# Performance work log

Measured on AMD Instinct MI355X. Metric: run time of the kernel, lower is better.

The kernel has to match this reference:

```python
import jax, jax.numpy as jnp
import numpy as np

B = 65536          # bs * m
N_NODES = 2        # fixed by module usage (job-machine pair graphs)
IN_FEAT = 256
N_HEADS = 4
N_HIDDEN = 256     # concat=False -> n_hidden = out_features
SLOPE = 0.2


def setup_inputs() -> dict:
    key = jax.random.key(0)
    k_h, k_adj, k_w, k_a = jax.random.split(key, 4)
    h = jax.random.normal(k_h, (B, N_NODES, IN_FEAT), dtype=jnp.float32)
    # adjacency: ij=1 means edge j->i; force self-loops on the diagonal
    adj = jax.random.randint(k_adj, (B, 1, N_NODES, N_NODES), 0, 2, dtype=jnp.int32)
    diag = jnp.arange(N_NODES)
    adj = adj.at[..., diag, diag].set(1)
    # xavier-normal-ish scales
    W = jax.random.normal(k_w, (IN_FEAT, N_HIDDEN * N_HEADS), dtype=jnp.float32) * (2.0 / (IN_FEAT + N_HIDDEN * N_HEADS)) ** 0.5
    a = jax.random.normal(k_a, (N_HEADS, 2 * N_HIDDEN, 1), dtype=jnp.float32) * (2.0 / (2 * N_HIDDEN + 1)) ** 0.5
    return {"h": h, "adj_mat": adj, "W": W, "a": a}


def reference(h, adj_mat, W, a):
    # h: (B, N, F_in); W: (F_in, H*D); a: (H, 2D, 1); adj_mat: (B, 1, N, N)
    Bsz, n_nodes, _ = h.shape
    n_heads = a.shape[0]
    n_hidden = a.shape[1] // 2
    # (B, N, H*D) -> (B, H, N, D)
    ht = (h @ W).reshape(Bsz, n_nodes, n_heads, n_hidden).transpose(0, 2, 1, 3)
    # attention scores: e[b,h,i,j] = leakyrelu(src[b,h,i] + tgt[b,h,j])
    src = jnp.einsum('bhnd,hd->bhn', ht, a[:, :n_hidden, 0])
    tgt = jnp.einsum('bhnd,hd->bhn', ht, a[:, n_hidden:, 0])
    e = jax.nn.leaky_relu(src[..., :, None] + tgt[..., None, :], SLOPE)
    e = jnp.where(adj_mat > 0, e, -jnp.inf)  # (B, H, N, N)
    attn = jax.nn.softmax(e, axis=-1)
    h_prime = jnp.einsum('bhij,bhjd->bhid', attn, ht)  # (B, H, N, D)
    # concat=False -> mean over heads
    return h_prime.mean(axis=1)  # (B, N, D)
```

## Files before the change

kernel.cpp:

```cpp
#include <hip/hip_runtime.h>
#include <hip/hip_bf16.h>


typedef __attribute__((ext_vector_type(8))) short short8;
typedef __attribute__((ext_vector_type(4))) float floatx4;

__device__ __forceinline__ float bf2f(short u) {
    union { unsigned int i; float f; } v;
    v.i = ((unsigned int)(unsigned short)u) << 16;
    return v.f;
}
__device__ __forceinline__ unsigned int pk2(float lo, float hi) {
    __hip_bfloat162 t = __float22bfloat162_rn(make_float2(lo, hi));
    union { __hip_bfloat162 h; unsigned int u; } cv; cv.h = t;
    return cv.u;
}

__global__ void gat_prep(const float* __restrict__ W, const float* __restrict__ a,
                         __hip_bfloat16* __restrict__ PT,
                         __hip_bfloat16* __restrict__ Wt2) {
    int b = blockIdx.x;
    if (b < 1024) {
        int idx = b * 256 + threadIdx.x;
        int d = idx & 255, hh = (idx >> 8) & 3, k = idx >> 10;
        int j = k >> 5, kl = k & 31;
        Wt2[(((hh * 8 + j) * 256 + d) << 5) + kl] =
            __float2bfloat16(W[k * 1024 + hh * 256 + d]);
    } else {
        int wid = (b - 1024) * 4 + (threadIdx.x >> 6);
        int lane = threadIdx.x & 63;
        int k = wid & 255, h = (wid >> 8) & 3, half = wid >> 10;
        float4 wv = *(const float4*)(W + k * 1024 + h * 256 + lane * 4);
        float4 av = *(const float4*)(a + h * 512 + half * 256 + lane * 4);
        float s = wv.x * av.x + wv.y * av.y + wv.z * av.z + wv.w * av.w;
        #pragma unroll
        for (int off = 32; off; off >>= 1) s += __shfl_down(s, off);
        if (lane == 0) PT[(half * 4 + h) * 256 + k] = __float2bfloat16(s);
        if (lane == 1) PT[2048 + wid] = __float2bfloat16(0.f);
    }
}

#define TB 32
#define ROWS 64

__global__ __launch_bounds__(256, 3)
void gat_main(const float* __restrict__ hin,
              const int* __restrict__ adj,
              const __hip_bfloat16* __restrict__ PT,
              const __hip_bfloat16* __restrict__ Wt2,
              float* __restrict__ out) {
    __shared__ __align__(16) short sH[ROWS * 256];
    __shared__ __align__(16) short sZd[2][ROWS * 64];
    __shared__ __align__(16) float2 sC[TB * 4 * 2];
    float (*sS)[16] = (float (*)[16])(&sZd[1][0]);

    const int tid = threadIdx.x;
    const int lane = tid & 63;
    const int wave = tid >> 6;
    const int m = lane & 15;
    const int q = lane >> 4;
    const long batch0 = (long)blockIdx.x * TB;
    char* sHb = (char*)sH;
    char* sZb = (char*)sZd;

    short8 ptf[8];
    {
        const short* ptg = (const short*)PT;
        #pragma unroll
        for (int ks = 0; ks < 8; ++ks)
            ptf[ks] = *(const short8*)(ptg + m * 256 + ks * 32 + q * 8);
    }
    int4 av = ((const int4*)adj)[batch0 + (tid >> 3)];

    {
        const float4* gh = (const float4*)(hin + batch0 * 512);
        #pragma unroll
        for (int it = 0; it < 16; ++it) {
            int idx = tid + it * 256;
            int r = idx >> 6, c4 = idx & 63;
            float4 v = gh[idx];
            uint2 bv;
            bv.x = pk2(v.x, v.y);
            bv.y = pk2(v.z, v.w);
            *(uint2*)(sHb + r * 512 + ((c4 * 8) ^ ((r & 7) << 4))) = bv;
        }
    }
    __syncthreads();

    {
        int row = wave * 16 + m;
        floatx4 a0 = {0.f, 0.f, 0.f, 0.f};
        #pragma unroll
        for (int ks = 0; ks < 8; ++ks) {
            short8 f0 = *(const short8*)(sHb + row * 512 +
                          ((ks * 64 + q * 16) ^ ((row & 7) << 4)));
            a0 = __builtin_amdgcn_mfma_f32_16x16x32_bf16(f0, ptf[ks], a0, 0, 0, 0);
        }
        #pragma unroll
        for (int r = 0; r < 4; ++r)
            sS[wave * 16 + q * 4 + r][m] = a0[r];
    }
    __syncthreads();

    {
        int lb = tid >> 3, hh = (tid >> 1) & 3, i = tid & 1;
        int m0 = i ? av.z : av.x, m1 = i ? av.w : av.y;
        float s  = sS[lb * 2 + i][hh];
        float t0 = sS[lb * 2][4 + hh], t1 = sS[lb * 2 + 1][4 + hh];
        float e0 = s + t0; e0 = e0 >= 0.f ? e0 : 0.2f * e0;
        float e1 = s + t1; e1 = e1 >= 0.f ? e1 : 0.2f * e1;
        e0 = fminf(fmaxf(e0, -80.f), 80.f);
        e1 = fminf(fmaxf(e1, -80.f), 80.f);
        bool k0 = m0 > 0, k1 = m1 > 0;
        float f0 = k0 ? e0 : -1e30f, f1 = k1 ? e1 : -1e30f;
        float mx = fmaxf(f0, f1);
        float p0 = k0 ? __expf(e0 - mx) : 0.f;
        float p1 = k1 ? __expf(e1 - mx) : 0.f;
        float den = p0 + p1;
        float inv = den > 1e-30f ? 0.25f / den : 0.f;
        sC[(lb * 4 + hh) * 2 + i] = make_float2(p0 * inv, p1 * inv);
    }
    __syncthreads();

    const int zg = tid & 7, zrb = tid >> 3;

    #define ZBUILD(ch, buf)                                                     \
    {                                                                           \
        int hh_ = (ch) >> 2, kc_ = (ch) & 3;                                    \
        _Pragma("unroll")                                                       \
        for (int half = 0; half < 2; ++half) {                                  \
            int zr = zrb + half * 32;                                           \
            float2 c = sC[((zr >> 1) * 4 + hh_) * 2 + (zr & 1)];                \
            int hr = zr & ~1;                                                   \
            int co = kc_ * 128 + zg * 16;                                       \
            short8 v0 = *(const short8*)(sHb + hr * 512 + (co ^ ((hr & 7) << 4))); \
            short8 v1 = *(const short8*)(sHb + (hr + 1) * 512 + (co ^ (((hr + 1) & 7) << 4))); \
            int4 zv; int* zp = (int*)&zv;                                       \
            _Pragma("unroll")                                                   \
            for (int jj = 0; jj < 4; ++jj) {                                    \
                float z0 = c.x * bf2f(v0[jj * 2])     + c.y * bf2f(v1[jj * 2]); \
                float z1 = c.x * bf2f(v0[jj * 2 + 1]) + c.y * bf2f(v1[jj * 2 + 1]); \
                zp[jj] = (int)pk2(z0, z1);                                      \
            }                                                                   \
            *(int4*)(sZb + (buf) * 8192 + zr * 128 + ((zg * 16) ^ ((zr & 7) << 4))) = zv; \
        }                                                                       \
    }

    floatx4 acc[4][4];
    #pragma unroll
    for (int i = 0; i < 4; ++i)
        #pragma unroll
        for (int j = 0; j < 4; ++j)
            acc[i][j] = (floatx4){0.f, 0.f, 0.f, 0.f};

    ZBUILD(0, 0);
    __syncthreads();

    int cur = 0;
    #pragma unroll 1
    for (int ch = 0; ch < 16; ++ch) {
        short8 bfr[2][4];
        {
            int hh = ch >> 2, kc = ch & 3;
            #pragma unroll
            for (int ks = 0; ks < 2; ++ks) {
                const short* wb = (const short*)Wt2 +
                    (((hh * 8 + kc * 2 + ks) * 256 + wave * 64 + m) << 5) + q * 8;
                #pragma unroll
                for (int nt = 0; nt < 4; ++nt)
                    bfr[ks][nt] = *(const short8*)(wb + (nt << 9));
            }
        }
        if (ch < 15) ZBUILD(ch + 1, cur ^ 1);
        #pragma unroll
        for (int ks = 0; ks < 2; ++ks)
            #pragma unroll
            for (int mt = 0; mt < 4; ++mt) {
                int row = mt * 16 + m;
                short8 af = *(const short8*)(sZb + cur * 8192 + row * 128 +
                              ((ks * 64 + q * 16) ^ ((row & 7) << 4)));
                #pragma unroll
                for (int nt = 0; nt < 4; ++nt)
                    acc[mt][nt] = __builtin_amdgcn_mfma_f32_16x16x32_bf16(
                        af, bfr[ks][nt], acc[mt][nt], 0, 0, 0);
            }
        __syncthreads();
        cur ^= 1;
    }

    {
        float* og = out + batch0 * 512;
        #pragma unroll
        for (int mt = 0; mt < 4; ++mt)
            #pragma unroll
            for (int nt = 0; nt < 4; ++nt) {
                int col = wave * 64 + nt * 16 + m;
                #pragma unroll
                for (int r = 0; r < 4; ++r)
                    og[(mt * 16 + q * 4 + r) * 256 + col] = acc[mt][nt][r];
            }
    }
    #undef ZBUILD
}

extern "C" void kernel_launch(void* const* d_in, const int* in_sizes, int n_in,
                              void* d_out, int out_size, void* d_ws, size_t ws_size,
                              hipStream_t stream) {
    const float* hin = (const float*)d_in[0];
    const int* adj   = (const int*)d_in[1];
    const float* W   = (const float*)d_in[2];
    const float* a   = (const float*)d_in[3];
    float* out       = (float*)d_out;

    __hip_bfloat16* PT  = (__hip_bfloat16*)d_ws;
    __hip_bfloat16* Wt2 = PT + 16 * 256;

    if (ws_size < (16 * 256 + 256 * 1024) * sizeof(__hip_bfloat16)) return;

    int B = in_sizes[0] / 512;
    gat_prep<<<1536, 256, 0, stream>>>(W, a, PT, Wt2);
    gat_main<<<B / TB, 256, 0, stream>>>(hin, adj, PT, Wt2, out);
}
```

Before: 291.3 us.

## Unroll main loop by two with register double-buffered weight fragments and lighter barriers

Unrolls the 16-chunk MFMA loop by two so the weight B-fragments for the next chunk are loaded into a second register set while the current chunk's MFMAs run, making the global-load latency overlap compute. The ping-pong LDS buffer index becomes a compile-time constant. __syncthreads is replaced with an explicit lgkmcnt wait plus s_barrier, which avoids waiting on outstanding global (vmcnt) loads at each barrier. Holding a second set of 8 short8 fragments raises register pressure under launch_bounds(256,3), which could cause spills or lower occupancy.

After: 342.5 us. +17.6%, slower.

```diff
diff --git a/kernel.cpp b/kernel.cpp
--- a/kernel.cpp
+++ b/kernel.cpp
@@ -62,6 +62,7 @@
     const long batch0 = (long)blockIdx.x * TB;
     char* sHb = (char*)sH;
     char* sZb = (char*)sZd;
+    const short* w2s = (const short*)Wt2;
 
     short8 ptf[8];
     {
@@ -146,6 +147,40 @@
         }                                                                       \
     }
 
+    #define LOADB(bfr, ch)                                                      \
+    {                                                                           \
+        int hh_ = (ch) >> 2, kc_ = (ch) & 3;                                    \
+        _Pragma("unroll")                                                       \
+        for (int ks = 0; ks < 2; ++ks) {                                        \
+            const short* wb = w2s +                                             \
+                (((hh_ * 8 + kc_ * 2 + ks) * 256 + wave * 64 + m) << 5) + q * 8;\
+            _Pragma("unroll")                                                   \
+            for (int nt = 0; nt < 4; ++nt)                                      \
+                bfr[ks * 4 + nt] = *(const short8*)(wb + (nt << 9));            \
+        }                                                                       \
+    }
+
+    #define MMASTEP(bfr, BUF)                                                   \
+    {                                                                           \
+        _Pragma("unroll")                                                       \
+        for (int ks = 0; ks < 2; ++ks)                                          \
+            _Pragma("unroll")                                                   \
+            for (int mt = 0; mt < 4; ++mt) {                                    \
+                int row = mt * 16 + m;                                          \
+                short8 af = *(const short8*)(sZb + (BUF) * 8192 + row * 128 +   \
+                              ((ks * 64 + q * 16) ^ ((row & 7) << 4)));         \
+                _Pragma("unroll")                                               \
+                for (int nt = 0; nt < 4; ++nt)                                  \
+                    acc[mt][nt] = __builtin_amdgcn_mfma_f32_16x16x32_bf16(      \
+                        af, bfr[ks * 4 + nt], acc[mt][nt], 0, 0, 0);            \
+            }                                                                   \
+    }
+
+    #define LOOPBAR()                                                           \
+        asm volatile("s_waitcnt lgkmcnt(0)" ::: "memory");                      \
+        __builtin_amdgcn_s_barrier();                                           \
+        asm volatile("" ::: "memory");
+
     floatx4 acc[4][4];
     #pragma unroll
     for (int i = 0; i < 4; ++i)
@@ -153,39 +188,25 @@
         for (int j = 0; j < 4; ++j)
             acc[i][j] = (floatx4){0.f, 0.f, 0.f, 0.f};
 
+    short8 bfrA[8], bfrB[8];
+
+    LOADB(bfrA, 0);
     ZBUILD(0, 0);
     __syncthreads();
 
-    int cur = 0;
     #pragma unroll 1
-    for (int ch = 0; ch < 16; ++ch) {
-        short8 bfr[2][4];
-        {
-            int hh = ch >> 2, kc = ch & 3;
-            #pragma unroll
-            for (int ks = 0; ks < 2; ++ks) {
-                const short* wb = (const short*)Wt2 +
-                    (((hh * 8 + kc * 2 + ks) * 256 + wave * 64 + m) << 5) + q * 8;
-                #pragma unroll
-                for (int nt = 0; nt < 4; ++nt)
-                    bfr[ks][nt] = *(const short8*)(wb + (nt << 9));
-            }
+    for (int ch2 = 0; ch2 < 8; ++ch2) {
+        int ch = ch2 * 2;
+        LOADB(bfrB, ch + 1);
+        ZBUILD(ch + 1, 1);
+        MMASTEP(bfrA, 0);
+        LOOPBAR();
+        if (ch2 < 7) {
+            LOADB(bfrA, ch + 2);
+            ZBUILD(ch + 2, 0);
         }
-        if (ch < 15) ZBUILD(ch + 1, cur ^ 1);
-        #pragma unroll
-        for (int ks = 0; ks < 2; ++ks)
-            #pragma unroll
-            for (int mt = 0; mt < 4; ++mt) {
-                int row = mt * 16 + m;
-                short8 af = *(const short8*)(sZb + cur * 8192 + row * 128 +
-                              ((ks * 64 + q * 16) ^ ((row & 7) << 4)));
-                #pragma unroll
-                for (int nt = 0; nt < 4; ++nt)
-                    acc[mt][nt] = __builtin_amdgcn_mfma_f32_16x16x32_bf16(
-                        af, bfr[ks][nt], acc[mt][nt], 0, 0, 0);
-            }
-        __syncthreads();
-        cur ^= 1;
+        MMASTEP(bfrB, 1);
+        LOOPBAR();
     }
 
     {
@@ -201,6 +222,9 @@
             }
     }
     #undef ZBUILD
+    #undef LOADB
+    #undef MMASTEP
+    #undef LOOPBAR
 }
 
 extern "C" void kernel_launch(void* const* d_in, const int* in_sizes, int n_in,
```
